# Kernel tuning notes

Hardware: AMD Instinct MI355X
Metric: run time of the kernel (lower is better)

Reference implementation:

```python
import jax, jax.numpy as jnp
import numpy as np

B, T, D = 16, 4096, 256
CODEBOOK_SIZE = 1024
COMMITMENT = 1.0


def setup_inputs() -> dict:
    key = jax.random.key(0)
    kx, kc = jax.random.split(key)
    x = jax.random.normal(kx, (B, T, D), dtype=jnp.float32)
    codebook = jax.random.normal(kc, (CODEBOOK_SIZE, D), dtype=jnp.float32)
    return {"x": x, "codebook": codebook}


def reference(x, codebook):
    # x: [B, T, D] continuous latents; codebook: [K, D]
    flat = x.reshape(-1, x.shape[-1])  # [N, D]
    # does not affect argmin but is kept for faithfulness to torch.cdist-style math)
    x_sq = jnp.sum(flat * flat, axis=1, keepdims=True)            # [N, 1]
    c_sq = jnp.sum(codebook * codebook, axis=1)                   # [K]
    dist = x_sq - 2.0 * (flat @ codebook.T) + c_sq[None, :]       # [N, K]
    indices = jnp.argmin(dist, axis=1)                            # [N] int
    quantized = codebook[indices].reshape(x.shape)                # gather, [B, T, D]
    # commitment loss: encoder pulled toward (stopped) codes
    commit_loss = COMMITMENT * jnp.mean(
        (x - jax.lax.stop_gradient(quantized)) ** 2
    )
    # straight-through estimator
    out = x + jax.lax.stop_gradient(quantized - x)
    return out, indices.reshape(x.shape[:-1]), commit_loss
```

## Files before the change

kernel.cpp:

```cpp
#include <hip/hip_runtime.h>

#define N_TOK 65536
#define DIM   256
#define KCODE 1024

#define NTHREADS 256
#define TM 128
#define TN 128
#define BK 32
#define NCHUNK 8
#define NSTAGE 24
#define OTM 128

#define REFINE_EPS 0.125f
#define TIE_THETA 1.0e-4

#define WS_CSQ_OFF   16
#define WS_IDX_OFF   2048
#define WS_PAIRS_OFF (WS_IDX_OFF + N_TOK)
#define WS_CBPK_OFF  (WS_PAIRS_OFF + N_TOK * NCHUNK * 4)

typedef float f32x4  __attribute__((ext_vector_type(4)));
typedef short bf16x8 __attribute__((ext_vector_type(8)));
typedef short s16x8  __attribute__((ext_vector_type(8)));

__global__ void rowsq_np_kernel(const float* __restrict__ m,
                                float* __restrict__ out,
                                float* __restrict__ loss_ws, int rows) {
#pragma clang fp contract(off)
    if (blockIdx.x == 0 && threadIdx.x == 0) loss_ws[0] = 0.0f;
    int row = blockIdx.x * 16 + (threadIdx.x >> 4);
    int l   = threadIdx.x & 15;
    if (row >= rows) return;
    int h = l >> 3;
    int j = l & 7;
    const float* p = m + (size_t)row * DIM + h * 128 + j;
    float v = p[0];
    float r = v * v;
#pragma unroll
    for (int i = 1; i < 16; ++i) {
        float w  = p[i * 8];
        float w2 = w * w;
        r = r + w2;
    }
    float t = r + __shfl_xor(r, 1);
    t = t + __shfl_xor(t, 2);
    t = t + __shfl_xor(t, 4);
    t = t + __shfl_xor(t, 8);
    if (l == 0) out[row] = t;
}

__device__ __forceinline__ void ins2(float d, int idx,
                                     float& d1, int& i1, float& d2, int& i2) {
    if (d < d1 || (d == d1 && idx < i1)) {
        d2 = d1; i2 = i1; d1 = d; i1 = idx;
    } else if ((d < d2 || (d == d2 && idx < i2)) && idx != i1) {
        d2 = d; i2 = idx;
    }
}

__device__ __forceinline__ void f2bf_split(float v, short& hi, short& lo) {
    unsigned u = __float_as_uint(v);
    unsigned r = (u + 0x7fffu + ((u >> 16) & 1u)) >> 16;
    hi = (short)r;
    float hf = __uint_as_float(r << 16);
    float lf = v - hf;
    unsigned u2 = __float_as_uint(lf);
    unsigned r2 = (u2 + 0x7fffu + ((u2 >> 16) & 1u)) >> 16;
    lo = (short)r2;
}

__global__ void pack_tiles_kernel(const float* __restrict__ src,
                                  unsigned short* __restrict__ dst,
                                  int total) {
    int tid = blockIdx.x * blockDim.x + threadIdx.x;
    if (tid >= total) return;
    int s   = tid & 3;
    int r   = (tid >> 2) & 127;
    int kc  = (tid >> 9) & 7;
    int g   = tid >> 12;
    int oct = s ^ ((r >> 1) & 3);

    const float4* xr = reinterpret_cast<const float4*>(
        src + ((size_t)(g * 128 + r)) * DIM + kc * 32 + oct * 8);
    float4 v0 = xr[0];
    float4 v1 = xr[1];

    float f[8] = {v0.x, v0.y, v0.z, v0.w, v1.x, v1.y, v1.z, v1.w};
    s16x8 hv, lv;
#pragma unroll
    for (int i = 0; i < 8; ++i) {
        short h, l;
        f2bf_split(f[i], h, l);
        hv[i] = h; lv[i] = l;
    }
    size_t base_hi = (((size_t)(g * 16 + kc) * 128 + r) << 5) + s * 8;
    size_t base_lo = (((size_t)(g * 16 + 8 + kc) * 128 + r) << 5) + s * 8;
    *reinterpret_cast<s16x8*>(dst + base_hi) = hv;
    *reinterpret_cast<s16x8*>(dst + base_lo) = lv;
}

__device__ __forceinline__ void gload_lds16(const unsigned short* g, unsigned short* lds) {
    __builtin_amdgcn_global_load_lds(
        (const __attribute__((address_space(1))) unsigned int*)g,
        (__attribute__((address_space(3))) unsigned int*)lds, 16, 0, 0);
}

__launch_bounds__(NTHREADS, 5)
__global__ void vq_main_kernel(const unsigned short* __restrict__ xpk,
                               const unsigned short* __restrict__ cbpk,
                               const float* __restrict__ csq,
                               float4* __restrict__ pairs) {
    __shared__ __align__(16) unsigned short shbuf[2][2 * TM * BK];

    const int tid  = threadIdx.x;
    const int w    = tid >> 6;
    const int wy   = w >> 1;
    const int wx   = w & 1;
    const int lane = tid & 63;
    const int lm   = lane & 15;
    const int q    = lane >> 4;

    const int bx     = blockIdx.x;
    const int jj     = bx >> 3;
    const int grp    = (bx & 7) + ((jj >> 3) << 3);
    const int cchunk = jj & 7;
    const int tok0   = grp * TM;
    const int code0  = cchunk * TN;

    float cs_reg[4];
#pragma unroll
    for (int ni = 0; ni < 4; ++ni)
        cs_reg[ni] = csq[code0 + wx * 64 + ni * 16 + lm];

    f32x4 acc[4][4];
#pragma unroll
    for (int mi = 0; mi < 4; ++mi)
#pragma unroll
        for (int ni = 0; ni < 4; ++ni)
            acc[mi][ni] = (f32x4){0.f, 0.f, 0.f, 0.f};

    int offA[4], offB[4];
#pragma unroll
    for (int mi = 0; mi < 4; ++mi) {
        int r = wy * 64 + mi * 16 + lm;
        offA[mi] = r * BK + ((q ^ ((r >> 1) & 3)) * 8);
    }
#pragma unroll
    for (int ni = 0; ni < 4; ++ni) {
        int r = wx * 64 + ni * 16 + lm;
        offB[ni] = TM * BK + r * BK + ((q ^ ((r >> 1) & 3)) * 8);
    }

    const int lsrc = w * 1024 + lane * 8;
    auto stage = [&](int p, int s) {
        const int seg = s >> 3;
        const int kc  = s & 7;
        const int pa  = (seg == 2) ? 8 : 0;
        const int pb  = (seg == 1) ? 8 : 0;
        const unsigned short* ga = xpk  + (((size_t)(grp    * 16 + pa + kc)) << 12) + lsrc;
        const unsigned short* gb = cbpk + (((size_t)(cchunk * 16 + pb + kc)) << 12) + lsrc;
        unsigned short* At = &shbuf[p][w * 1024];
        unsigned short* Bt = &shbuf[p][TM * BK + w * 1024];
        gload_lds16(ga,       At);
        gload_lds16(ga + 512, At + 512);
        gload_lds16(gb,       Bt);
        gload_lds16(gb + 512, Bt + 512);
    };

    stage(0, 0);
    __syncthreads();

    int p = 0;
#pragma unroll 1
    for (int s = 0; s < NSTAGE; ++s) {
        if (s < NSTAGE - 1) stage(p ^ 1, s + 1);

        const unsigned short* buf = &shbuf[p][0];
        bf16x8 af[4], bf[4];
#pragma unroll
        for (int mi = 0; mi < 4; ++mi)
            af[mi] = *reinterpret_cast<const bf16x8*>(buf + offA[mi]);
#pragma unroll
        for (int ni = 0; ni < 4; ++ni)
            bf[ni] = *reinterpret_cast<const bf16x8*>(buf + offB[ni]);

#pragma unroll
        for (int mi = 0; mi < 4; ++mi)
#pragma unroll
            for (int ni = 0; ni < 4; ++ni)
                acc[mi][ni] = __builtin_amdgcn_mfma_f32_16x16x32_bf16(
                    af[mi], bf[ni], acc[mi][ni], 0, 0, 0);

        __syncthreads();
        p ^= 1;
    }

    float4 (*pairs_sh)[2] = reinterpret_cast<float4(*)[2]>(&shbuf[0][0]);

#pragma unroll
    for (int mi = 0; mi < 4; ++mi) {
#pragma unroll
        for (int r = 0; r < 4; ++r) {
            int row_local = wy * 64 + mi * 16 + q * 4 + r;
            float l1 = 3.4e38f, l2 = 3.4e38f;
            int   j1 = 0x7fffffff, j2 = 0x7fffffff;
#pragma unroll
            for (int ni = 0; ni < 4; ++ni) {
                float d = cs_reg[ni] - 2.0f * acc[mi][ni][r];
                ins2(d, code0 + wx * 64 + ni * 16 + lm, l1, j1, l2, j2);
            }
#pragma unroll
            for (int m = 1; m < 16; m <<= 1) {
                float o1 = __shfl_xor(l1, m);
                int   p1 = __shfl_xor(j1, m);
                float o2 = __shfl_xor(l2, m);
                int   p2 = __shfl_xor(j2, m);
                ins2(o1, p1, l1, j1, l2, j2);
                ins2(o2, p2, l1, j1, l2, j2);
            }
            if (lm == 0) {
                float4 pr;
                pr.x = l1; pr.y = l2;
                pr.z = __int_as_float(j1); pr.w = __int_as_float(j2);
                pairs_sh[row_local][wx] = pr;
            }
        }
    }
    __syncthreads();
    if (tid < TM) {
        float4 pa = pairs_sh[tid][0];
        float4 pb = pairs_sh[tid][1];
        float d1 = pa.x, d2 = pa.y;
        int   i1 = __float_as_int(pa.z), i2 = __float_as_int(pa.w);
        ins2(pb.x, __float_as_int(pb.z), d1, i1, d2, i2);
        ins2(pb.y, __float_as_int(pb.w), d1, i1, d2, i2);
        float4 pr;
        pr.x = d1; pr.y = d2;
        pr.z = __int_as_float(i1); pr.w = __int_as_float(i2);
        pairs[(size_t)cchunk * N_TOK + tok0 + tid] = pr;
    }
}

__launch_bounds__(256)
__global__ void merge_output_kernel(const float* __restrict__ x,
                                    const float* __restrict__ cb,
                                    const float4* __restrict__ pairs,
                                    float* __restrict__ out_q,
                                    float* __restrict__ out_idx,
                                    float* __restrict__ loss_ws) {
    __shared__ int   sh_idx[OTM];
    __shared__ float wsum[4];
    const int tid  = threadIdx.x;
    const int tok0 = blockIdx.x * OTM;

    if (tid < OTM) {
        const int t = tok0 + tid;
        float4 p0 = pairs[t];
        float d1 = p0.x, d2 = p0.y;
        int   i1 = __float_as_int(p0.z), i2 = __float_as_int(p0.w);
#pragma unroll
        for (int c = 1; c < NCHUNK; ++c) {
            float4 p = pairs[(size_t)c * N_TOK + t];
            ins2(p.x, __float_as_int(p.z), d1, i1, d2, i2);
            ins2(p.y, __float_as_int(p.w), d1, i1, d2, i2);
        }

        int pick = i1;
        if (d2 - d1 < REFINE_EPS) {
            const float* xr = x + (size_t)t * DIM;
            const float* c1 = cb + (size_t)i1 * DIM;
            const float* c2 = cb + (size_t)i2 * DIM;
            double sA = 0.0, dA = 0.0, sB = 0.0, dB = 0.0;
            for (int k = 0; k < DIM; ++k) {
                double xv = (double)xr[k];
                double a  = (double)c1[k];
                double b  = (double)c2[k];
                sA += a * a; dA += xv * a;
                sB += b * b; dB += xv * b;
            }
            double DA  = sA - 2.0 * dA;
            double DB  = sB - 2.0 * dB;
            double gap = DB - DA;
            if (gap > TIE_THETA)       pick = i1;
            else if (gap < -TIE_THETA) pick = i2;
            else                       pick = (i1 < i2) ? i1 : i2;
        }
        sh_idx[tid] = pick;
        out_idx[t]  = (float)pick;
    }
    __syncthreads();

    float lsum = 0.0f;
    for (int t = 0; t < OTM; ++t) {
        int code = sh_idx[t];
        float qv = cb[(size_t)code * DIM + tid];
        float xv = x[(size_t)(tok0 + t) * DIM + tid];
        out_q[(size_t)(tok0 + t) * DIM + tid] = xv + (qv - xv);
        float df = xv - qv;
        lsum = fmaf(df, df, lsum);
    }

#pragma unroll
    for (int off = 1; off < 64; off <<= 1) lsum += __shfl_xor(lsum, off);
    if ((tid & 63) == 0) wsum[tid >> 6] = lsum;
    __syncthreads();
    if (tid == 0) atomicAdd(loss_ws, (wsum[0] + wsum[1]) + (wsum[2] + wsum[3]));
}

__global__ void finalize_kernel(const float* ws, float* out_loss) {
    if (threadIdx.x == 0) out_loss[0] = ws[0] * (1.0f / 16777216.0f);
}

extern "C" void kernel_launch(void* const* d_in, const int* in_sizes, int n_in,
                              void* d_out, int out_size, void* d_ws, size_t ws_size,
                              hipStream_t stream) {
    const float* x  = (const float*)d_in[0];
    const float* cb = (const float*)d_in[1];

    float* out      = (float*)d_out;
    float* out_q    = out;
    float* out_idx  = out + (size_t)N_TOK * DIM;
    float* out_loss = out_idx + N_TOK;

    float*  ws    = (float*)d_ws;
    float*  csq   = ws + WS_CSQ_OFF;
    float4* pairs = (float4*)(ws + WS_PAIRS_OFF);
    unsigned short* cbpk = (unsigned short*)(ws + WS_CBPK_OFF);
    unsigned short* xpk  = (unsigned short*)out_q;

    rowsq_np_kernel<<<KCODE / 16, 256, 0, stream>>>(cb, csq, ws, KCODE);
    pack_tiles_kernel<<<(N_TOK * 32) / 256, 256, 0, stream>>>(x, xpk, N_TOK * 32);
    pack_tiles_kernel<<<(KCODE * 32) / 256, 256, 0, stream>>>(cb, cbpk, KCODE * 32);
    vq_main_kernel<<<(N_TOK / TM) * NCHUNK, NTHREADS, 0, stream>>>(xpk, cbpk, csq, pairs);
    merge_output_kernel<<<N_TOK / OTM, 256, 0, stream>>>(x, cb, pairs, out_q, out_idx, ws);
    finalize_kernel<<<1, 64, 0, stream>>>(ws, out_loss);
}
```

Before: 798.8 us.

## Enlarge distance GEMM tiles to 256x256 with 512-thread blocks

Result: slower. 1.798 ms (+125.1%).

```diff
diff --git a/kernel.cpp b/kernel.cpp
--- a/kernel.cpp
+++ b/kernel.cpp
@@ -4,11 +4,11 @@
 #define DIM   256
 #define KCODE 1024
 
-#define NTHREADS 256
-#define TM 128
-#define TN 128
+#define NTHREADS 512
+#define BM 256
+#define BN 256
 #define BK 32
-#define NCHUNK 8
+#define NCHUNK 4
 #define NSTAGE 24
 #define OTM 128
 
@@ -18,7 +18,7 @@
 #define WS_CSQ_OFF   16
 #define WS_IDX_OFF   2048
 #define WS_PAIRS_OFF (WS_IDX_OFF + N_TOK)
-#define WS_CBPK_OFF  (WS_PAIRS_OFF + N_TOK * NCHUNK * 4)
+#define WS_CBPK_OFF  (WS_PAIRS_OFF + N_TOK * 8 * 4)
 
 typedef float f32x4  __attribute__((ext_vector_type(4)));
 typedef short bf16x8 __attribute__((ext_vector_type(8)));
@@ -76,13 +76,13 @@
     int tid = blockIdx.x * blockDim.x + threadIdx.x;
     if (tid >= total) return;
     int s   = tid & 3;
-    int r   = (tid >> 2) & 127;
-    int kc  = (tid >> 9) & 7;
-    int g   = tid >> 12;
+    int r   = (tid >> 2) & 255;
+    int kc  = (tid >> 10) & 7;
+    int g   = tid >> 13;
     int oct = s ^ ((r >> 1) & 3);
 
     const float4* xr = reinterpret_cast<const float4*>(
-        src + ((size_t)(g * 128 + r)) * DIM + kc * 32 + oct * 8);
+        src + ((size_t)(g * 256 + r)) * DIM + kc * 32 + oct * 8);
     float4 v0 = xr[0];
     float4 v1 = xr[1];
 
@@ -94,8 +94,8 @@
         f2bf_split(f[i], h, l);
         hv[i] = h; lv[i] = l;
     }
-    size_t base_hi = (((size_t)(g * 16 + kc) * 128 + r) << 5) + s * 8;
-    size_t base_lo = (((size_t)(g * 16 + 8 + kc) * 128 + r) << 5) + s * 8;
+    size_t base_hi = ((size_t)(g * 16 + kc)     * 8192) + r * 32 + s * 8;
+    size_t base_lo = ((size_t)(g * 16 + 8 + kc) * 8192) + r * 32 + s * 8;
     *reinterpret_cast<s16x8*>(dst + base_hi) = hv;
     *reinterpret_cast<s16x8*>(dst + base_lo) = lv;
 }
@@ -106,50 +106,50 @@
         (__attribute__((address_space(3))) unsigned int*)lds, 16, 0, 0);
 }
 
-__launch_bounds__(NTHREADS, 5)
+__launch_bounds__(NTHREADS, 1)
 __global__ void vq_main_kernel(const unsigned short* __restrict__ xpk,
                                const unsigned short* __restrict__ cbpk,
                                const float* __restrict__ csq,
                                float4* __restrict__ pairs) {
-    __shared__ __align__(16) unsigned short shbuf[2][2 * TM * BK];
+    __shared__ __align__(16) unsigned short shbuf[2][2 * BM * BK];
 
     const int tid  = threadIdx.x;
     const int w    = tid >> 6;
-    const int wy   = w >> 1;
-    const int wx   = w & 1;
+    const int wy   = w >> 2;
+    const int wx   = w & 3;
     const int lane = tid & 63;
     const int lm   = lane & 15;
     const int q    = lane >> 4;
 
-    const int bx     = blockIdx.x;
-    const int jj     = bx >> 3;
-    const int grp    = (bx & 7) + ((jj >> 3) << 3);
-    const int cchunk = jj & 7;
-    const int tok0   = grp * TM;
-    const int code0  = cchunk * TN;
+    const int bx    = blockIdx.x;
+    const int swz   = (bx & 7) * 128 + (bx >> 3);
+    const int grp   = swz >> 2;
+    const int nb    = swz & 3;
+    const int tok0  = grp * BM;
+    const int code0 = nb * BN;
 
     float cs_reg[4];
 #pragma unroll
     for (int ni = 0; ni < 4; ++ni)
         cs_reg[ni] = csq[code0 + wx * 64 + ni * 16 + lm];
 
-    f32x4 acc[4][4];
-#pragma unroll
-    for (int mi = 0; mi < 4; ++mi)
+    f32x4 acc[8][4];
+#pragma unroll
+    for (int mi = 0; mi < 8; ++mi)
 #pragma unroll
         for (int ni = 0; ni < 4; ++ni)
             acc[mi][ni] = (f32x4){0.f, 0.f, 0.f, 0.f};
 
-    int offA[4], offB[4];
-#pragma unroll
-    for (int mi = 0; mi < 4; ++mi) {
-        int r = wy * 64 + mi * 16 + lm;
+    int offA[8], offB[4];
+#pragma unroll
+    for (int mi = 0; mi < 8; ++mi) {
+        int r = wy * 128 + mi * 16 + lm;
         offA[mi] = r * BK + ((q ^ ((r >> 1) & 3)) * 8);
     }
 #pragma unroll
     for (int ni = 0; ni < 4; ++ni) {
         int r = wx * 64 + ni * 16 + lm;
-        offB[ni] = TM * BK + r * BK + ((q ^ ((r >> 1) & 3)) * 8);
+        offB[ni] = BM * BK + r * BK + ((q ^ ((r >> 1) & 3)) * 8);
     }
 
     const int lsrc = w * 1024 + lane * 8;
@@ -158,10 +158,10 @@
         const int kc  = s & 7;
         const int pa  = (seg == 2) ? 8 : 0;
         const int pb  = (seg == 1) ? 8 : 0;
-        const unsigned short* ga = xpk  + (((size_t)(grp    * 16 + pa + kc)) << 12) + lsrc;
-        const unsigned short* gb = cbpk + (((size_t)(cchunk * 16 + pb + kc)) << 12) + lsrc;
+        const unsigned short* ga = xpk  + ((size_t)(grp * 16 + pa + kc) * 8192) + lsrc;
+        const unsigned short* gb = cbpk + ((size_t)(nb  * 16 + pb + kc) * 8192) + lsrc;
         unsigned short* At = &shbuf[p][w * 1024];
-        unsigned short* Bt = &shbuf[p][TM * BK + w * 1024];
+        unsigned short* Bt = &shbuf[p][BM * BK + w * 1024];
         gload_lds16(ga,       At);
         gload_lds16(ga + 512, At + 512);
         gload_lds16(gb,       Bt);
@@ -177,16 +177,16 @@
         if (s < NSTAGE - 1) stage(p ^ 1, s + 1);
 
         const unsigned short* buf = &shbuf[p][0];
-        bf16x8 af[4], bf[4];
-#pragma unroll
-        for (int mi = 0; mi < 4; ++mi)
+        bf16x8 af[8], bf[4];
+#pragma unroll
+        for (int mi = 0; mi < 8; ++mi)
             af[mi] = *reinterpret_cast<const bf16x8*>(buf + offA[mi]);
 #pragma unroll
         for (int ni = 0; ni < 4; ++ni)
             bf[ni] = *reinterpret_cast<const bf16x8*>(buf + offB[ni]);
 
 #pragma unroll
-        for (int mi = 0; mi < 4; ++mi)
+        for (int mi = 0; mi < 8; ++mi)
 #pragma unroll
             for (int ni = 0; ni < 4; ++ni)
                 acc[mi][ni] = __builtin_amdgcn_mfma_f32_16x16x32_bf16(
@@ -196,18 +196,18 @@
         p ^= 1;
     }
 
-    float4 (*pairs_sh)[2] = reinterpret_cast<float4(*)[2]>(&shbuf[0][0]);
-
-#pragma unroll
-    for (int mi = 0; mi < 4; ++mi) {
-#pragma unroll
-        for (int r = 0; r < 4; ++r) {
-            int row_local = wy * 64 + mi * 16 + q * 4 + r;
+    float4 (*pairs_sh)[4] = reinterpret_cast<float4(*)[4]>(&shbuf[0][0]);
+
+#pragma unroll
+    for (int mi = 0; mi < 8; ++mi) {
+#pragma unroll
+        for (int rr = 0; rr < 4; ++rr) {
+            int row_local = wy * 128 + mi * 16 + q * 4 + rr;
             float l1 = 3.4e38f, l2 = 3.4e38f;
             int   j1 = 0x7fffffff, j2 = 0x7fffffff;
 #pragma unroll
             for (int ni = 0; ni < 4; ++ni) {
-                float d = cs_reg[ni] - 2.0f * acc[mi][ni][r];
+                float d = cs_reg[ni] - 2.0f * acc[mi][ni][rr];
                 ins2(d, code0 + wx * 64 + ni * 16 + lm, l1, j1, l2, j2);
             }
 #pragma unroll
@@ -228,17 +228,20 @@
         }
     }
     __syncthreads();
-    if (tid < TM) {
-        float4 pa = pairs_sh[tid][0];
-        float4 pb = pairs_sh[tid][1];
-        float d1 = pa.x, d2 = pa.y;
-        int   i1 = __float_as_int(pa.z), i2 = __float_as_int(pa.w);
-        ins2(pb.x, __float_as_int(pb.z), d1, i1, d2, i2);
-        ins2(pb.y, __float_as_int(pb.w), d1, i1, d2, i2);
+    if (tid < BM) {
+        float4 p0 = pairs_sh[tid][0];
+        float d1 = p0.x, d2 = p0.y;
+        int   i1 = __float_as_int(p0.z), i2 = __float_as_int(p0.w);
+#pragma unroll
+        for (int c = 1; c < 4; ++c) {
+            float4 pc = pairs_sh[tid][c];
+            ins2(pc.x, __float_as_int(pc.z), d1, i1, d2, i2);
+            ins2(pc.y, __float_as_int(pc.w), d1, i1, d2, i2);
+        }
         float4 pr;
         pr.x = d1; pr.y = d2;
         pr.z = __int_as_float(i1); pr.w = __int_as_float(i2);
-        pairs[(size_t)cchunk * N_TOK + tok0 + tid] = pr;
+        pairs[(size_t)nb * N_TOK + tok0 + tid] = pr;
     }
 }
 
@@ -332,7 +335,7 @@
     rowsq_np_kernel<<<KCODE / 16, 256, 0, stream>>>(cb, csq, ws, KCODE);
     pack_tiles_kernel<<<(N_TOK * 32) / 256, 256, 0, stream>>>(x, xpk, N_TOK * 32);
     pack_tiles_kernel<<<(KCODE * 32) / 256, 256, 0, stream>>>(cb, cbpk, KCODE * 32);
-    vq_main_kernel<<<(N_TOK / TM) * NCHUNK, NTHREADS, 0, stream>>>(xpk, cbpk, csq, pairs);
+    vq_main_kernel<<<(N_TOK / BM) * NCHUNK, NTHREADS, 0, stream>>>(xpk, cbpk, csq, pairs);
     merge_output_kernel<<<N_TOK / OTM, 256, 0, stream>>>(x, cb, pairs, out_q, out_idx, ws);
     finalize_kernel<<<1, 64, 0, stream>>>(ws, out_loss);
 }
```

## Preload full x tile into LDS once and stream only codebook stages

Applied to the files above, without the earlier changes.

New measurement: 1.466 ms. 1.84x slower.

```diff
diff --git a/kernel.cpp b/kernel.cpp
--- a/kernel.cpp
+++ b/kernel.cpp
@@ -11,6 +11,9 @@
 #define NCHUNK 8
 #define NSTAGE 24
 #define OTM 128
+
+#define LDS_SHORTS (65536 + 2 * 4096)
+#define LDS_BYTES  (LDS_SHORTS * 2)
 
 #define REFINE_EPS 0.125f
 #define TIE_THETA 1.0e-4
@@ -106,12 +109,12 @@
         (__attribute__((address_space(3))) unsigned int*)lds, 16, 0, 0);
 }
 
-__launch_bounds__(NTHREADS, 5)
+__launch_bounds__(NTHREADS, 1)
 __global__ void vq_main_kernel(const unsigned short* __restrict__ xpk,
                                const unsigned short* __restrict__ cbpk,
                                const float* __restrict__ csq,
                                float4* __restrict__ pairs) {
-    __shared__ __align__(16) unsigned short shbuf[2][2 * TM * BK];
+    extern __shared__ __align__(16) unsigned short sh[];
 
     const int tid  = threadIdx.x;
     const int w    = tid >> 6;
@@ -149,41 +152,50 @@
 #pragma unroll
     for (int ni = 0; ni < 4; ++ni) {
         int r = wx * 64 + ni * 16 + lm;
-        offB[ni] = TM * BK + r * BK + ((q ^ ((r >> 1) & 3)) * 8);
+        offB[ni] = r * BK + ((q ^ ((r >> 1) & 3)) * 8);
+    }
+
+    {
+        const unsigned short* gaBase = xpk + ((size_t)grp << 16);
+        const int lofs = w * 512 + lane * 8;
+#pragma unroll
+        for (int i = 0; i < 32; ++i)
+            gload_lds16(gaBase + i * 2048 + lofs, &sh[i * 2048 + w * 512]);
     }
 
     const int lsrc = w * 1024 + lane * 8;
-    auto stage = [&](int p, int s) {
+    auto stageB = [&](int p, int s) {
+        const int seg = s >> 3;
+        const int kc  = s & 7;
+        const int pb  = (seg == 1) ? 8 : 0;
+        const unsigned short* gb =
+            cbpk + (((size_t)(cchunk * 16 + pb + kc)) << 12) + lsrc;
+        unsigned short* Bt = &sh[65536 + p * 4096 + w * 1024];
+        gload_lds16(gb,       Bt);
+        gload_lds16(gb + 512, Bt + 512);
+    };
+
+    stageB(0, 0);
+    __syncthreads();
+
+    int p = 0;
+#pragma unroll 1
+    for (int s = 0; s < NSTAGE; ++s) {
+        if (s < NSTAGE - 1) stageB(p ^ 1, s + 1);
+
         const int seg = s >> 3;
         const int kc  = s & 7;
         const int pa  = (seg == 2) ? 8 : 0;
-        const int pb  = (seg == 1) ? 8 : 0;
-        const unsigned short* ga = xpk  + (((size_t)(grp    * 16 + pa + kc)) << 12) + lsrc;
-        const unsigned short* gb = cbpk + (((size_t)(cchunk * 16 + pb + kc)) << 12) + lsrc;
-        unsigned short* At = &shbuf[p][w * 1024];
-        unsigned short* Bt = &shbuf[p][TM * BK + w * 1024];
-        gload_lds16(ga,       At);
-        gload_lds16(ga + 512, At + 512);
-        gload_lds16(gb,       Bt);
-        gload_lds16(gb + 512, Bt + 512);
-    };
-
-    stage(0, 0);
-    __syncthreads();
-
-    int p = 0;
-#pragma unroll 1
-    for (int s = 0; s < NSTAGE; ++s) {
-        if (s < NSTAGE - 1) stage(p ^ 1, s + 1);
-
-        const unsigned short* buf = &shbuf[p][0];
+        const unsigned short* aChunk = &sh[(pa + kc) * 4096];
+        const unsigned short* bBuf   = &sh[65536 + p * 4096];
+
         bf16x8 af[4], bf[4];
 #pragma unroll
         for (int mi = 0; mi < 4; ++mi)
-            af[mi] = *reinterpret_cast<const bf16x8*>(buf + offA[mi]);
+            af[mi] = *reinterpret_cast<const bf16x8*>(aChunk + offA[mi]);
 #pragma unroll
         for (int ni = 0; ni < 4; ++ni)
-            bf[ni] = *reinterpret_cast<const bf16x8*>(buf + offB[ni]);
+            bf[ni] = *reinterpret_cast<const bf16x8*>(bBuf + offB[ni]);
 
 #pragma unroll
         for (int mi = 0; mi < 4; ++mi)
@@ -196,7 +208,7 @@
         p ^= 1;
     }
 
-    float4 (*pairs_sh)[2] = reinterpret_cast<float4(*)[2]>(&shbuf[0][0]);
+    float4 (*pairs_sh)[2] = reinterpret_cast<float4(*)[2]>(&sh[0]);
 
 #pragma unroll
     for (int mi = 0; mi < 4; ++mi) {
@@ -332,7 +344,8 @@
     rowsq_np_kernel<<<KCODE / 16, 256, 0, stream>>>(cb, csq, ws, KCODE);
     pack_tiles_kernel<<<(N_TOK * 32) / 256, 256, 0, stream>>>(x, xpk, N_TOK * 32);
     pack_tiles_kernel<<<(KCODE * 32) / 256, 256, 0, stream>>>(cb, cbpk, KCODE * 32);
-    vq_main_kernel<<<(N_TOK / TM) * NCHUNK, NTHREADS, 0, stream>>>(xpk, cbpk, csq, pairs);
+    vq_main_kernel<<<(N_TOK / TM) * NCHUNK, NTHREADS, LDS_BYTES, stream>>>(
+        xpk, cbpk, csq, pairs);
     merge_output_kernel<<<N_TOK / OTM, 256, 0, stream>>>(x, cb, pairs, out_q, out_idx, ws);
     finalize_kernel<<<1, 64, 0, stream>>>(ws, out_loss);
 }
```
